# Kernel optimization log

Hardware: AMD Instinct MI355X
Metric: run time of the kernel (lower is better)

The kernel has to match this reference:

```python
import jax, jax.numpy as jnp
import numpy as np

B, N, DIM, H, DH = 2, 2048, 256, 8, 32
DIM_INNER = H * DH  # 256


def setup_inputs() -> dict:
    key = jax.random.key(0)
    ks = jax.random.split(key, 8)
    s = DIM ** -0.5  # keep activations / logits in a sane range
    return {
        "x_real": jax.random.normal(ks[0], (B, N, DIM), jnp.float32),
        "x_imag": jax.random.normal(ks[1], (B, N, DIM), jnp.float32),
        "wq_r": jax.random.normal(ks[2], (DIM, DIM_INNER), jnp.float32) * s,
        "wq_i": jax.random.normal(ks[3], (DIM, DIM_INNER), jnp.float32) * s,
        "wkv_r": jax.random.normal(ks[4], (DIM, 2 * DIM_INNER), jnp.float32) * s,
        "wkv_i": jax.random.normal(ks[5], (DIM, 2 * DIM_INNER), jnp.float32) * s,
        "wo_r": jax.random.normal(ks[6], (DIM_INNER, DIM), jnp.float32) * s,
        "wo_i": jax.random.normal(ks[7], (DIM_INNER, DIM), jnp.float32) * s,
    }


def _clin(xr, xi, wr, wi):
    # complex linear: (xr + i xi) @ (wr + i wi)
    return xr @ wr - xi @ wi, xr @ wi + xi @ wr


def _split_heads(t):
    b, n, _ = t.shape
    return t.reshape(b, n, H, DH).transpose(0, 2, 1, 3)  # b h n d


def _merge_heads(t):
    b, h, n, d = t.shape
    return t.transpose(0, 2, 1, 3).reshape(b, n, h * d)


def reference(x_real, x_imag, wq_r, wq_i, wkv_r, wkv_i, wo_r, wo_i):
    # complex projections
    qr, qi = _clin(x_real, x_imag, wq_r, wq_i)
    kvr, kvi = _clin(x_real, x_imag, wkv_r, wkv_i)
    kr, vr = jnp.split(kvr, 2, axis=-1)
    ki, vi = jnp.split(kvi, 2, axis=-1)
    qr, qi, kr, ki, vr, vi = map(_split_heads, (qr, qi, kr, ki, vr, vi))

    # complex_attention_complete (sec 3.2 eq 3): 4 real SDPA replicas.
    # q repeat '(c r b)' -> blocks [qr, qr, qi, qi]; k repeat '(r c b)' -> [kr, ki, kr, ki]
    scale = DH ** -0.5
    Q = jnp.stack([qr, qr, qi, qi])        # [4, b, h, n, d]
    K = jnp.stack([kr, ki, kr, ki])
    sim = jnp.einsum('rbhid,rbhjd->rbhij', Q, K) * scale
    A = jax.nn.softmax(sim, axis=-1)       # [4, b, h, n, n]

    av = lambda a, v: jnp.einsum('bhij,bhjd->bhid', a, v)
    # sign-recombine trick: indices [0,3,5,6 | 1,2,4,7], sign [[1,-1,-1,-1],[1,1,1,-1]]
    o_r = av(A[0], vr) - av(A[1], vi) - av(A[2], vi) - av(A[3], vr)
    o_i = av(A[0], vi) + av(A[1], vr) + av(A[2], vr) - av(A[3], vi)

    mr, mi = _merge_heads(o_r), _merge_heads(o_i)
    out_r, out_i = _clin(mr, mi, wo_r, wo_i)
    # real view of the complex output: [b, n, dim, 2]
    return jnp.stack([out_r, out_i], axis=-1)
```

## Files before the change

### kernel.cpp

```cpp
#include <hip/hip_runtime.h>
#include <math.h>

namespace {
constexpr int kB = 2, kN = 2048, kDim = 256, kH = 8, kDH = 32;
constexpr int kBH = kB * kH;
constexpr long kPlane = (long)kBH * kN * kDH;
constexpr float kQScaleL2 = 0.25506852552f;
}

typedef unsigned short u16;
typedef short short8 __attribute__((ext_vector_type(8)));
typedef short short4v __attribute__((ext_vector_type(4)));
typedef float floatx16 __attribute__((ext_vector_type(16)));
#define MFMA_BF16(a, b, c) __builtin_amdgcn_mfma_f32_32x32x16_bf16(a, b, c, 0, 0, 0)

__device__ inline u16 bf16b(float x) {
    union { float f; unsigned u; } c; c.f = x;
    unsigned r = c.u + 0x7FFFu + ((c.u >> 16) & 1u);
    return (u16)(r >> 16);
}
__device__ inline unsigned pack2(float x, float y) {
    return (unsigned)bf16b(x) | ((unsigned)bf16b(y) << 16);
}
__device__ inline unsigned packtr(float lo, float hi) {
    return __builtin_amdgcn_perm(__float_as_uint(hi), __float_as_uint(lo), 0x07060302u);
}
__device__ inline short8 mk8(const float* e) {
    union { unsigned u[4]; short8 s; } c;
    c.u[0] = packtr(e[0], e[1]);
    c.u[1] = packtr(e[2], e[3]);
    c.u[2] = packtr(e[4], e[5]);
    c.u[3] = packtr(e[6], e[7]);
    return c.s;
}

__global__ __launch_bounds__(256, 2) void prep_w(
    const float* __restrict__ wq_r, const float* __restrict__ wq_i,
    const float* __restrict__ wkv_r, const float* __restrict__ wkv_i,
    const float* __restrict__ wo_r, const float* __restrict__ wo_i,
    u16* __restrict__ Wbig, u16* __restrict__ WoT)
{
    const long base = ((long)blockIdx.x * 256 + threadIdx.x) * 4;
    if (base < 786432) {
        const int c = (int)(base >> 9);
        const int k = (int)(base & 511);
        const int g = c >> 8, d = c & 255;
        const bool hi = k >= 256;
        const int k2 = hi ? k - 256 : k;
        const float* src;
        float sgn = 1.f;
        int col, stride;
        if (g < 2) {
            stride = 256; col = d;
            if (g == 0) { src = hi ? wq_i : wq_r; if (hi) sgn = -1.f; }
            else        { src = hi ? wq_r : wq_i; }
            sgn *= kQScaleL2;
        } else {
            stride = 512;
            col = (g >= 4) ? d + 256 : d;
            if ((g & 1) == 0) { src = hi ? wkv_i : wkv_r; if (hi) sgn = -1.f; }
            else              { src = hi ? wkv_r : wkv_i; }
        }
        short4v v;
        #pragma unroll
        for (int j = 0; j < 4; ++j)
            v[j] = (short)bf16b(src[(long)(k2 + j) * stride + col] * sgn);
        *(short4v*)(Wbig + base) = v;
    } else {
        const long o = base - 786432;
        const int c = (int)(o >> 9);
        const int k = (int)(o & 511);
        const bool hi = k >= 256;
        const int k2 = hi ? k - 256 : k;
        const float* src;
        float sgn = 1.f;
        int col;
        if (c < 256) { col = c;       src = hi ? wo_i : wo_r; if (hi) sgn = -1.f; }
        else         { col = c - 256; src = hi ? wo_r : wo_i; }
        short4v v;
        #pragma unroll
        for (int j = 0; j < 4; ++j)
            v[j] = (short)bf16b(src[(long)(k2 + j) * 256 + col] * sgn);
        *(short4v*)(WoT + o) = v;
    }
}

__global__ __launch_bounds__(256, 2) void gemm_proj(
    const float* __restrict__ xr_g, const float* __restrict__ xi_g,
    const u16* __restrict__ BT,
    u16* __restrict__ qr, u16* __restrict__ qi, u16* __restrict__ kr,
    u16* __restrict__ ki, u16* __restrict__ vrT, u16* __restrict__ viT)
{
    __shared__ __align__(16) u16 sAB[8192];
    u16* sA = sAB;
    u16* sB = sAB + 4096;
    const int tid = threadIdx.x;
    const int lane = tid & 63, l31 = lane & 31, lh = lane >> 5;
    const int w = tid >> 6, wrow = w & 1, wcol = w >> 1;
    const int srow = tid >> 2, sseg = tid & 3;
    const int n0 = blockIdx.x * 128, m0 = blockIdx.y * 128;

    floatx16 a00 = {0}, a01 = {0}, a10 = {0}, a11 = {0};

    for (int kt = 0; kt < 512; kt += 32) {
        __syncthreads();
        const float* xbase = (kt < 256) ? xr_g : xi_g;
        const int kc = (kt & 255) + sseg * 8;
        #pragma unroll
        for (int i = 0; i < 2; ++i) {
            const int r = srow + i * 64;
            {
                const float* src = xbase + (long)(m0 + r) * 256 + kc;
                const float4 f0 = *(const float4*)(src);
                const float4 f1 = *(const float4*)(src + 4);
                short8 v;
                v[0] = (short)bf16b(f0.x); v[1] = (short)bf16b(f0.y);
                v[2] = (short)bf16b(f0.z); v[3] = (short)bf16b(f0.w);
                v[4] = (short)bf16b(f1.x); v[5] = (short)bf16b(f1.y);
                v[6] = (short)bf16b(f1.z); v[7] = (short)bf16b(f1.w);
                *(short8*)(sA + r * 32 + sseg * 8) = v;
            }
            *(short8*)(sB + r * 32 + sseg * 8) =
                *(const short8*)(BT + (long)(n0 + r) * 512 + kt + sseg * 8);
        }
        __syncthreads();
        #pragma unroll
        for (int s = 0; s < 2; ++s) {
            const int ko = s * 16 + lh * 8;
            const short8 fa0 = *(const short8*)(sA + (wrow * 64 + l31) * 32 + ko);
            const short8 fa1 = *(const short8*)(sA + (wrow * 64 + 32 + l31) * 32 + ko);
            const short8 fb0 = *(const short8*)(sB + (wcol * 64 + l31) * 32 + ko);
            const short8 fb1 = *(const short8*)(sB + (wcol * 64 + 32 + l31) * 32 + ko);
            a00 = MFMA_BF16(fa0, fb0, a00);
            a01 = MFMA_BF16(fa0, fb1, a01);
            a10 = MFMA_BF16(fa1, fb0, a10);
            a11 = MFMA_BF16(fa1, fb1, a11);
        }
    }

    __syncthreads();
    u16* scr = sAB + w * 1088;

    floatx16 accs[2][2] = {{a00, a01}, {a10, a11}};
    #pragma unroll
    for (int rt = 0; rt < 2; ++rt) {
        #pragma unroll
        for (int ct = 0; ct < 2; ++ct) {
            const int colb = n0 + wcol * 64 + ct * 32;
            const int g = colb >> 8;
            const int h = (colb & 255) >> 5;
            if (g < 4) {
                u16* pl = (g == 0) ? qr : (g == 1) ? qi : (g == 2) ? kr : ki;
                #pragma unroll
                for (int reg = 0; reg < 16; ++reg) {
                    const int row = m0 + wrow * 64 + rt * 32 + (reg & 3) + 8 * (reg >> 2) + 4 * lh;
                    const int b = row >> 11, nn = row & 2047;
                    pl[(((long)(b * 8 + h)) * 2048 + nn) * 32 + l31] = bf16b(accs[rt][ct][reg]);
                }
            } else {
                #pragma unroll
                for (int q = 0; q < 4; ++q) {
                    union { unsigned u[2]; uint2 v; } pk;
                    pk.u[0] = pack2(accs[rt][ct][4 * q + 0], accs[rt][ct][4 * q + 1]);
                    pk.u[1] = pack2(accs[rt][ct][4 * q + 2], accs[rt][ct][4 * q + 3]);
                    *(uint2*)(scr + l31 * 34 + 8 * q + 4 * lh) = pk.v;
                }
                asm volatile("s_waitcnt lgkmcnt(0)" ::: "memory");
                const int rowb = m0 + wrow * 64 + rt * 32;
                const int b_ = rowb >> 11, nnb = rowb & 2047;
                u16* plane = (g == 4) ? vrT : viT;
                u16* rowbase = plane + ((long)(b_ * 8 + h) * 32) * 2048 + nnb;
                const int p = lane & 15;
                const int sp = (p & ~6) | ((p & 2) << 1) | ((p & 4) >> 1);
                const int dgrp = lane >> 4;
                #pragma unroll
                for (int ds_ = 0; ds_ < 8; ++ds_) {
                    const int d = ds_ * 4 + dgrp;
                    const unsigned v = *(const unsigned*)(scr + d * 34 + 2 * sp);
                    *(unsigned*)(rowbase + (long)d * 2048 + 2 * p) = v;
                }
                asm volatile("s_waitcnt lgkmcnt(0)" ::: "memory");
            }
        }
    }
}

__global__ __launch_bounds__(256, 2) void attn_kernel(
    const u16* __restrict__ qr_g, const u16* __restrict__ qi_g,
    const u16* __restrict__ kr_g, const u16* __restrict__ ki_g,
    const u16* __restrict__ vrT_g, const u16* __restrict__ viT_g,
    u16* __restrict__ xo)
{
    __shared__ __align__(16) u16 smem[2][2][64 * 40];

    const int tid = threadIdx.x;
    const int lane = tid & 63, l31 = lane & 31, lh = lane >> 5;
    const int w = tid >> 6, strip = w & 1, qtype = w >> 1;
    const int bh = blockIdx.x;
    const int i0 = blockIdx.y * 64;
    const long base = (long)bh * kN * kDH;

    const u16* qg = (qtype ? qi_g : qr_g) + base;
    short8 qB0, qB1;
    {
        const u16* qp = qg + (long)(i0 + strip * 32 + l31) * kDH;
        qB0 = *(const short8*)(qp + lh * 8);
        qB1 = *(const short8*)(qp + 16 + lh * 8);
    }

    const int srow = tid & 63;
    const int sseg = tid >> 6;
    const u16* kptr = ((srow < 32) ? kr_g : ki_g) + base
                    + (long)(srow & 31) * kDH + sseg * 8;
    const u16* vptr = ((srow < 32) ? vrT_g : viT_g)
                    + ((long)bh * 32 + (srow & 31)) * kN + sseg * 8;

    short8 kreg = *(const short8*)kptr;
    short8 vreg = *(const short8*)vptr;

    floatx16 U0r = {0}, U0i = {0}, U1r = {0}, U1i = {0};
    float La0 = 0.f, La1 = 0.f;

    for (int t = 0; t < 64; ++t) {
        u16* bK = smem[0][t & 1];
        u16* bV = smem[1][t & 1];
        *(short8*)(bK + srow * 40 + sseg * 8) = kreg;
        *(short8*)(bV + srow * 40 + sseg * 8) = vreg;
        __syncthreads();
        if (t < 63) {
            kreg = *(const short8*)(kptr + (long)(t + 1) * 1024);
            vreg = *(const short8*)(vptr + (t + 1) * 32);
        }

        const short8 ka0 = *(const short8*)(bK + l31 * 40 + lh * 8);
        const short8 ka1 = *(const short8*)(bK + l31 * 40 + 16 + lh * 8);
        const short8 kb0 = *(const short8*)(bK + (32 + l31) * 40 + lh * 8);
        const short8 kb1 = *(const short8*)(bK + (32 + l31) * 40 + 16 + lh * 8);
        floatx16 S0 = {0}, S1 = {0};
        S0 = MFMA_BF16(ka0, qB0, S0);
        S0 = MFMA_BF16(ka1, qB1, S0);
        S1 = MFMA_BF16(kb0, qB0, S1);
        S1 = MFMA_BF16(kb1, qB1, S1);

        float e0[16], e1[16];
        #pragma unroll
        for (int r = 0; r < 16; ++r) {
            e0[r] = __builtin_amdgcn_exp2f(S0[r]);
            La0 += e0[r];
        }
        #pragma unroll
        for (int r = 0; r < 16; ++r) {
            e1[r] = __builtin_amdgcn_exp2f(S1[r]);
            La1 += e1[r];
        }
        const short8 F0a = mk8(&e0[0]);
        const short8 F0b = mk8(&e0[8]);
        const short8 F1a = mk8(&e1[0]);
        const short8 F1b = mk8(&e1[8]);

        const short8 va0 = *(const short8*)(bV + l31 * 40 + lh * 8);
        const short8 va1 = *(const short8*)(bV + l31 * 40 + 16 + lh * 8);
        const short8 vb0 = *(const short8*)(bV + (32 + l31) * 40 + lh * 8);
        const short8 vb1 = *(const short8*)(bV + (32 + l31) * 40 + 16 + lh * 8);

        U0r = MFMA_BF16(va0, F0a, U0r);
        U0r = MFMA_BF16(va1, F0b, U0r);
        U0i = MFMA_BF16(vb0, F0a, U0i);
        U0i = MFMA_BF16(vb1, F0b, U0i);
        U1r = MFMA_BF16(va0, F1a, U1r);
        U1r = MFMA_BF16(va1, F1b, U1r);
        U1i = MFMA_BF16(vb0, F1a, U1i);
        U1i = MFMA_BF16(vb1, F1b, U1i);
    }

    La0 += __shfl_xor(La0, 32);
    La1 += __shfl_xor(La1, 32);
    const float iL0 = 1.f / La0, iL1 = 1.f / La1;

    float po_r[16], po_i[16];
    #pragma unroll
    for (int r = 0; r < 16; ++r) {
        if (qtype == 0) {
            po_r[r] =  U0r[r] * iL0 - U1i[r] * iL1;
            po_i[r] =  U0i[r] * iL0 + U1r[r] * iL1;
        } else {
            po_r[r] = -U0i[r] * iL0 - U1r[r] * iL1;
            po_i[r] =  U0r[r] * iL0 - U1i[r] * iL1;
        }
    }

    __syncthreads();
    float* sC = (float*)smem;
    if (qtype == 1) {
        float* dst = sC + strip * (2 * 32 * 33);
        #pragma unroll
        for (int r = 0; r < 16; ++r) {
            const int d = (r & 3) + 8 * (r >> 2) + 4 * lh;
            dst[d * 33 + l31] = po_r[r];
            dst[32 * 33 + d * 33 + l31] = po_i[r];
        }
    }
    __syncthreads();
    if (qtype == 0) {
        const float* src = sC + strip * (2 * 32 * 33);
        const int b = bh >> 3, h = bh & 7;
        u16* xrow = xo + ((long)(b * 2048 + i0 + strip * 32 + l31)) * 512 + h * 32;
        #pragma unroll
        for (int g = 0; g < 4; ++g) {
            const int d0 = 8 * g + 4 * lh;
            union { unsigned u[2]; uint2 v; } pr, pi;
            pr.u[0] = pack2(po_r[4 * g + 0] + src[(d0 + 0) * 33 + l31],
                            po_r[4 * g + 1] + src[(d0 + 1) * 33 + l31]);
            pr.u[1] = pack2(po_r[4 * g + 2] + src[(d0 + 2) * 33 + l31],
                            po_r[4 * g + 3] + src[(d0 + 3) * 33 + l31]);
            pi.u[0] = pack2(po_i[4 * g + 0] + src[32 * 33 + (d0 + 0) * 33 + l31],
                            po_i[4 * g + 1] + src[32 * 33 + (d0 + 1) * 33 + l31]);
            pi.u[1] = pack2(po_i[4 * g + 2] + src[32 * 33 + (d0 + 2) * 33 + l31],
                            po_i[4 * g + 3] + src[32 * 33 + (d0 + 3) * 33 + l31]);
            *(uint2*)(xrow + d0) = pr.v;
            *(uint2*)(xrow + 256 + d0) = pi.v;
        }
    }
}

__global__ __launch_bounds__(256, 2) void gemm_oproj(
    const u16* __restrict__ Xo, const u16* __restrict__ BT, float* __restrict__ out)
{
    __shared__ __align__(16) u16 sA[128 * 32];
    __shared__ __align__(16) u16 sB[128 * 32];
    const int tid = threadIdx.x;
    const int lane = tid & 63, l31 = lane & 31, lh = lane >> 5;
    const int w = tid >> 6, wrow = w & 1, wcol = w >> 1;
    const int srow = tid >> 2, sseg = tid & 3;
    const int n0 = blockIdx.x * 128, m0 = blockIdx.y * 128;

    floatx16 a00 = {0}, a01 = {0}, a10 = {0}, a11 = {0};

    for (int kt = 0; kt < 512; kt += 32) {
        __syncthreads();
        #pragma unroll
        for (int i = 0; i < 2; ++i) {
            const int r = srow + i * 64;
            *(short8*)(sA + r * 32 + sseg * 8) =
                *(const short8*)(Xo + (long)(m0 + r) * 512 + kt + sseg * 8);
            *(short8*)(sB + r * 32 + sseg * 8) =
                *(const short8*)(BT + (long)(n0 + r) * 512 + kt + sseg * 8);
        }
        __syncthreads();
        #pragma unroll
        for (int s = 0; s < 2; ++s) {
            const int ko = s * 16 + lh * 8;
            const short8 fa0 = *(const short8*)(sA + (wrow * 64 + l31) * 32 + ko);
            const short8 fa1 = *(const short8*)(sA + (wrow * 64 + 32 + l31) * 32 + ko);
            const short8 fb0 = *(const short8*)(sB + (wcol * 64 + l31) * 32 + ko);
            const short8 fb1 = *(const short8*)(sB + (wcol * 64 + 32 + l31) * 32 + ko);
            a00 = MFMA_BF16(fa0, fb0, a00);
            a01 = MFMA_BF16(fa0, fb1, a01);
            a10 = MFMA_BF16(fa1, fb0, a10);
            a11 = MFMA_BF16(fa1, fb1, a11);
        }
    }

    floatx16 accs[2][2] = {{a00, a01}, {a10, a11}};
    #pragma unroll
    for (int rt = 0; rt < 2; ++rt) {
        #pragma unroll
        for (int ct = 0; ct < 2; ++ct) {
            const int colb = n0 + wcol * 64 + ct * 32;
            #pragma unroll
            for (int reg = 0; reg < 16; ++reg) {
                const int row = m0 + wrow * 64 + rt * 32 + (reg & 3) + 8 * (reg >> 2) + 4 * lh;
                const int col = colb + l31;
                const float val = accs[rt][ct][reg];
                if (colb < 256) out[(long)row * 512 + col * 2] = val;
                else            out[(long)row * 512 + (col - 256) * 2 + 1] = val;
            }
        }
    }
}

extern "C" void kernel_launch(void* const* d_in, const int* in_sizes, int n_in,
                              void* d_out, int out_size, void* d_ws, size_t ws_size,
                              hipStream_t stream) {
    const float* xr    = (const float*)d_in[0];
    const float* xi    = (const float*)d_in[1];
    const float* wq_r  = (const float*)d_in[2];
    const float* wq_i  = (const float*)d_in[3];
    const float* wkv_r = (const float*)d_in[4];
    const float* wkv_i = (const float*)d_in[5];
    const float* wo_r  = (const float*)d_in[6];
    const float* wo_i  = (const float*)d_in[7];
    float* out = (float*)d_out;

    u16* ws16 = (u16*)d_ws;
    u16* qr   = ws16 + 0 * kPlane;
    u16* qi   = ws16 + 1 * kPlane;
    u16* kr   = ws16 + 2 * kPlane;
    u16* ki   = ws16 + 3 * kPlane;
    u16* vrT  = ws16 + 4 * kPlane;
    u16* viT  = ws16 + 5 * kPlane;
    u16* xo   = ws16 + 6 * kPlane;
    u16* Wbig = ws16 + 8 * kPlane;
    u16* WoT  = Wbig + 786432;

    prep_w<<<1024, 256, 0, stream>>>(wq_r, wq_i, wkv_r, wkv_i, wo_r, wo_i, Wbig, WoT);
    gemm_proj<<<dim3(12, 32), 256, 0, stream>>>(xr, xi, Wbig, qr, qi, kr, ki, vrT, viT);
    attn_kernel<<<dim3(kBH, kN / 64), 256, 0, stream>>>(qr, qi, kr, ki, vrT, viT, xo);
    gemm_oproj<<<dim3(4, 32), 256, 0, stream>>>(xo, WoT, out);
}
```

Before: 170.9 us.

## Pre-convert X to bf16, double-buffer GEMMs with direct global-to-LDS loads

The input x is now converted to bf16 once, inside the weight prep kernel, and stored in the xo workspace buffer. The projection GEMM then streams bf16 tiles with global_load_lds into double-buffered shared memory, so the next tile loads while the current one is computed, with one barrier per step. The output GEMM gets smaller 64x64 tiles for more blocks, the same double buffering, and an interleaved WoT column layout so results store straight into the real/imag interleaved output. This adds a larger prep kernel and an extra bf16 copy of x. It relies on xo being free until the attention kernel overwrites it.

```diff
diff --git a/kernel.cpp b/kernel.cpp
--- a/kernel.cpp
+++ b/kernel.cpp
@@ -33,12 +33,18 @@
     c.u[3] = packtr(e[6], e[7]);
     return c.s;
 }
+__device__ inline void gload16(const u16* g, u16* l) {
+    __builtin_amdgcn_global_load_lds(
+        (const __attribute__((address_space(1))) void*)g,
+        (__attribute__((address_space(3))) void*)l, 16, 0, 0);
+}
 
 __global__ __launch_bounds__(256, 2) void prep_w(
+    const float* __restrict__ xr_g, const float* __restrict__ xi_g,
     const float* __restrict__ wq_r, const float* __restrict__ wq_i,
     const float* __restrict__ wkv_r, const float* __restrict__ wkv_i,
     const float* __restrict__ wo_r, const float* __restrict__ wo_i,
-    u16* __restrict__ Wbig, u16* __restrict__ WoT)
+    u16* __restrict__ Wbig, u16* __restrict__ WoT, u16* __restrict__ Xbf)
 {
     const long base = ((long)blockIdx.x * 256 + threadIdx.x) * 4;
     if (base < 786432) {
@@ -66,71 +72,74 @@
         for (int j = 0; j < 4; ++j)
             v[j] = (short)bf16b(src[(long)(k2 + j) * stride + col] * sgn);
         *(short4v*)(Wbig + base) = v;
-    } else {
+    } else if (base < 1048576) {
         const long o = base - 786432;
         const int c = (int)(o >> 9);
         const int k = (int)(o & 511);
         const bool hi = k >= 256;
         const int k2 = hi ? k - 256 : k;
+        const int col = c >> 1;
         const float* src;
         float sgn = 1.f;
-        int col;
-        if (c < 256) { col = c;       src = hi ? wo_i : wo_r; if (hi) sgn = -1.f; }
-        else         { col = c - 256; src = hi ? wo_r : wo_i; }
+        if ((c & 1) == 0) { src = hi ? wo_i : wo_r; if (hi) sgn = -1.f; }
+        else              { src = hi ? wo_r : wo_i; }
         short4v v;
         #pragma unroll
         for (int j = 0; j < 4; ++j)
             v[j] = (short)bf16b(src[(long)(k2 + j) * 256 + col] * sgn);
         *(short4v*)(WoT + o) = v;
+    } else {
+        const long o = base - 1048576;
+        const int row = (int)(o >> 9);
+        const int col = (int)(o & 511);
+        const float* src = (col < 256) ? (xr_g + (long)row * 256 + col)
+                                       : (xi_g + (long)row * 256 + col - 256);
+        const float4 f = *(const float4*)src;
+        short4v v;
+        v[0] = (short)bf16b(f.x); v[1] = (short)bf16b(f.y);
+        v[2] = (short)bf16b(f.z); v[3] = (short)bf16b(f.w);
+        *(short4v*)(Xbf + o) = v;
     }
 }
 
 __global__ __launch_bounds__(256, 2) void gemm_proj(
-    const float* __restrict__ xr_g, const float* __restrict__ xi_g,
-    const u16* __restrict__ BT,
+    const u16* __restrict__ Xbf, const u16* __restrict__ BT,
     u16* __restrict__ qr, u16* __restrict__ qi, u16* __restrict__ kr,
     u16* __restrict__ ki, u16* __restrict__ vrT, u16* __restrict__ viT)
 {
-    __shared__ __align__(16) u16 sAB[8192];
-    u16* sA = sAB;
-    u16* sB = sAB + 4096;
+    __shared__ __align__(16) u16 sA[2][128 * 32];
+    __shared__ __align__(16) u16 sB[2][128 * 32];
     const int tid = threadIdx.x;
     const int lane = tid & 63, l31 = lane & 31, lh = lane >> 5;
     const int w = tid >> 6, wrow = w & 1, wcol = w >> 1;
-    const int srow = tid >> 2, sseg = tid & 3;
     const int n0 = blockIdx.x * 128, m0 = blockIdx.y * 128;
 
+    const int rb0 = w * 32;
+    const int grow = lane >> 2;
+    const int gseg = (lane & 3) * 8;
+
+    auto stage = [&](int b, int kt) {
+        #pragma unroll
+        for (int half = 0; half < 2; ++half) {
+            const int r = rb0 + half * 16;
+            gload16(Xbf + (long)(m0 + r + grow) * 512 + kt + gseg, &sA[b][r * 32]);
+            gload16(BT + (long)(n0 + r + grow) * 512 + kt + gseg, &sB[b][r * 32]);
+        }
+    };
+
     floatx16 a00 = {0}, a01 = {0}, a10 = {0}, a11 = {0};
-
-    for (int kt = 0; kt < 512; kt += 32) {
+    stage(0, 0);
+    for (int it = 0; it < 16; ++it) {
+        const int cur = it & 1;
         __syncthreads();
-        const float* xbase = (kt < 256) ? xr_g : xi_g;
-        const int kc = (kt & 255) + sseg * 8;
-        #pragma unroll
-        for (int i = 0; i < 2; ++i) {
-            const int r = srow + i * 64;
-            {
-                const float* src = xbase + (long)(m0 + r) * 256 + kc;
-                const float4 f0 = *(const float4*)(src);
-                const float4 f1 = *(const float4*)(src + 4);
-                short8 v;
-                v[0] = (short)bf16b(f0.x); v[1] = (short)bf16b(f0.y);
-                v[2] = (short)bf16b(f0.z); v[3] = (short)bf16b(f0.w);
-                v[4] = (short)bf16b(f1.x); v[5] = (short)bf16b(f1.y);
-                v[6] = (short)bf16b(f1.z); v[7] = (short)bf16b(f1.w);
-                *(short8*)(sA + r * 32 + sseg * 8) = v;
-            }
-            *(short8*)(sB + r * 32 + sseg * 8) =
-                *(const short8*)(BT + (long)(n0 + r) * 512 + kt + sseg * 8);
-        }
-        __syncthreads();
+        if (it < 15) stage(cur ^ 1, (it + 1) * 32);
         #pragma unroll
         for (int s = 0; s < 2; ++s) {
             const int ko = s * 16 + lh * 8;
-            const short8 fa0 = *(const short8*)(sA + (wrow * 64 + l31) * 32 + ko);
-            const short8 fa1 = *(const short8*)(sA + (wrow * 64 + 32 + l31) * 32 + ko);
-            const short8 fb0 = *(const short8*)(sB + (wcol * 64 + l31) * 32 + ko);
-            const short8 fb1 = *(const short8*)(sB + (wcol * 64 + 32 + l31) * 32 + ko);
+            const short8 fa0 = *(const short8*)(&sA[cur][(wrow * 64 + l31) * 32 + ko]);
+            const short8 fa1 = *(const short8*)(&sA[cur][(wrow * 64 + 32 + l31) * 32 + ko]);
+            const short8 fb0 = *(const short8*)(&sB[cur][(wcol * 64 + l31) * 32 + ko]);
+            const short8 fb1 = *(const short8*)(&sB[cur][(wcol * 64 + 32 + l31) * 32 + ko]);
             a00 = MFMA_BF16(fa0, fb0, a00);
             a01 = MFMA_BF16(fa0, fb1, a01);
             a10 = MFMA_BF16(fa1, fb0, a10);
@@ -139,7 +148,7 @@
     }
 
     __syncthreads();
-    u16* scr = sAB + w * 1088;
+    u16* scr = ((u16*)sA) + w * 1088;
 
     floatx16 accs[2][2] = {{a00, a01}, {a10, a11}};
     #pragma unroll
@@ -326,56 +335,42 @@
 __global__ __launch_bounds__(256, 2) void gemm_oproj(
     const u16* __restrict__ Xo, const u16* __restrict__ BT, float* __restrict__ out)
 {
-    __shared__ __align__(16) u16 sA[128 * 32];
-    __shared__ __align__(16) u16 sB[128 * 32];
+    __shared__ __align__(16) u16 sA[2][64 * 32];
+    __shared__ __align__(16) u16 sB[2][64 * 32];
     const int tid = threadIdx.x;
     const int lane = tid & 63, l31 = lane & 31, lh = lane >> 5;
     const int w = tid >> 6, wrow = w & 1, wcol = w >> 1;
-    const int srow = tid >> 2, sseg = tid & 3;
-    const int n0 = blockIdx.x * 128, m0 = blockIdx.y * 128;
-
-    floatx16 a00 = {0}, a01 = {0}, a10 = {0}, a11 = {0};
-
-    for (int kt = 0; kt < 512; kt += 32) {
+    const int n0 = blockIdx.x * 64, m0 = blockIdx.y * 64;
+
+    const int rb0 = w * 16;
+    const int grow = lane >> 2;
+    const int gseg = (lane & 3) * 8;
+
+    auto stage = [&](int b, int kt) {
+        gload16(Xo + (long)(m0 + rb0 + grow) * 512 + kt + gseg, &sA[b][rb0 * 32]);
+        gload16(BT + (long)(n0 + rb0 + grow) * 512 + kt + gseg, &sB[b][rb0 * 32]);
+    };
+
+    floatx16 acc = {0};
+    stage(0, 0);
+    for (int it = 0; it < 16; ++it) {
+        const int cur = it & 1;
         __syncthreads();
-        #pragma unroll
-        for (int i = 0; i < 2; ++i) {
-            const int r = srow + i * 64;
-            *(short8*)(sA + r * 32 + sseg * 8) =
-                *(const short8*)(Xo + (long)(m0 + r) * 512 + kt + sseg * 8);
-            *(short8*)(sB + r * 32 + sseg * 8) =
-                *(const short8*)(BT + (long)(n0 + r) * 512 + kt + sseg * 8);
-        }
-        __syncthreads();
+        if (it < 15) stage(cur ^ 1, (it + 1) * 32);
         #pragma unroll
         for (int s = 0; s < 2; ++s) {
             const int ko = s * 16 + lh * 8;
-            const short8 fa0 = *(const short8*)(sA + (wrow * 64 + l31) * 32 + ko);
-            const short8 fa1 = *(const short8*)(sA + (wrow * 64 + 32 + l31) * 32 + ko);
-            const short8 fb0 = *(const short8*)(sB + (wcol * 64 + l31) * 32 + ko);
-            const short8 fb1 = *(const short8*)(sB + (wcol * 64 + 32 + l31) * 32 + ko);
-            a00 = MFMA_BF16(fa0, fb0, a00);
-            a01 = MFMA_BF16(fa0, fb1, a01);
-            a10 = MFMA_BF16(fa1, fb0, a10);
-            a11 = MFMA_BF16(fa1, fb1, a11);
-        }
-    }
-
-    floatx16 accs[2][2] = {{a00, a01}, {a10, a11}};
+            const short8 fa = *(const short8*)(&sA[cur][(wrow * 32 + l31) * 32 + ko]);
+            const short8 fb = *(const short8*)(&sB[cur][(wcol * 32 + l31) * 32 + ko]);
+            acc = MFMA_BF16(fa, fb, acc);
+        }
+    }
+
+    const int col = n0 + wcol * 32 + l31;
     #pragma unroll
-    for (int rt = 0; rt < 2; ++rt) {
-        #pragma unroll
-        for (int ct = 0; ct < 2; ++ct) {
-            const int colb = n0 + wcol * 64 + ct * 32;
-            #pragma unroll
-            for (int reg = 0; reg < 16; ++reg) {
-                const int row = m0 + wrow * 64 + rt * 32 + (reg & 3) + 8 * (reg >> 2) + 4 * lh;
-                const int col = colb + l31;
-                const float val = accs[rt][ct][reg];
-                if (colb < 256) out[(long)row * 512 + col * 2] = val;
-                else            out[(long)row * 512 + (col - 256) * 2 + 1] = val;
-            }
-        }
+    for (int reg = 0; reg < 16; ++reg) {
+        const int row = m0 + wrow * 32 + (reg & 3) + 8 * (reg >> 2) + 4 * lh;
+        out[(long)row * 512 + col] = acc[reg];
     }
 }
 
@@ -402,9 +397,11 @@
     u16* xo   = ws16 + 6 * kPlane;
     u16* Wbig = ws16 + 8 * kPlane;
     u16* WoT  = Wbig + 786432;
-
-    prep_w<<<1024, 256, 0, stream>>>(wq_r, wq_i, wkv_r, wkv_i, wo_r, wo_i, Wbig, WoT);
-    gemm_proj<<<dim3(12, 32), 256, 0, stream>>>(xr, xi, Wbig, qr, qi, kr, ki, vrT, viT);
+    u16* Xbf  = xo;
+
+    prep_w<<<3072, 256, 0, stream>>>(xr, xi, wq_r, wq_i, wkv_r, wkv_i, wo_r, wo_i,
+                                     Wbig, WoT, Xbf);
+    gemm_proj<<<dim3(12, 32), 256, 0, stream>>>(Xbf, Wbig, qr, qi, kr, ki, vrT, viT);
     attn_kernel<<<dim3(kBH, kN / 64), 256, 0, stream>>>(qr, qi, kr, ki, vrT, viT, xo);
-    gemm_oproj<<<dim3(4, 32), 256, 0, stream>>>(xo, WoT, out);
-}
+    gemm_oproj<<<dim3(8, 64), 256, 0, stream>>>(xo, WoT, out);
+}
```

New measurement: 168.0 us. About the same (-1.7%).
